# Performance work log

Hardware: AMD Instinct MI355X
Metric: run time of the kernel (lower is better)

## Reference

```python
import jax, jax.numpy as jnp
import numpy as np

N_NODES = 50000
N_GRAPHS = 2048
BN_EPS = 1e-5


def setup_inputs() -> dict:
    key = jax.random.key(0)
    ks = jax.random.split(key, 12)
    n_feat, dim, n_out, n_edges = 128, 128, 12, 800000
    x = jax.random.normal(ks[0], (N_NODES, n_feat), dtype=jnp.float32)
    edge_index = jax.random.randint(ks[1], (2, n_edges), 0, N_NODES, dtype=jnp.int32)
    batch = jnp.sort(jax.random.randint(ks[2], (N_NODES,), 0, N_GRAPHS, dtype=jnp.int32))
    def lin(k, fan_in, fan_out):
        bound = 1.0 / np.sqrt(fan_in)
        kw, kb = jax.random.split(k)
        W = jax.random.uniform(kw, (fan_in, fan_out), minval=-bound, maxval=bound, dtype=jnp.float32)
        b = jax.random.uniform(kb, (fan_out,), minval=-bound, maxval=bound, dtype=jnp.float32)
        return W, b
    W1, b1 = lin(ks[3], n_feat, dim)
    W2, b2 = lin(ks[4], dim, dim)
    gamma = jnp.ones((dim,), dtype=jnp.float32)
    beta = jnp.zeros((dim,), dtype=jnp.float32)
    Wf1, bf1 = lin(ks[5], dim, 2 * dim)
    Wf2, bf2 = lin(ks[6], 2 * dim, n_out)
    return {"x": x, "edge_index": edge_index, "batch": batch,
            "W1": W1, "b1": b1, "W2": W2, "b2": b2,
            "gamma": gamma, "beta": beta,
            "Wf1": Wf1, "bf1": bf1, "Wf2": Wf2, "bf2": bf2}


def reference(x, edge_index, batch, W1, b1, W2, b2, gamma, beta, Wf1, bf1, Wf2, bf2):
    src, dst = edge_index[0], edge_index[1]
    # GINConv (eps=0): h = nn1(x + sum_{j in N(i)} x_j), scatter-add at dst
    agg = jax.ops.segment_sum(x[src], dst, num_segments=N_NODES)  # [N, F]
    h = x + agg
    h = jax.nn.relu(h @ W1 + b1) @ W2 + b2  # nn1 MLP
    h = jax.nn.relu(h)
    # BatchNorm1d (training mode: batch statistics, biased variance)
    mean = jnp.mean(h, axis=0)
    var = jnp.mean((h - mean) ** 2, axis=0)
    h = (h - mean) * jax.lax.rsqrt(var + BN_EPS) * gamma + beta
    # global_add_pool over graphs
    g = jax.ops.segment_sum(h, batch, num_segments=N_GRAPHS)  # [G, dim]
    g = jax.nn.relu(g @ Wf1 + bf1)
    return g @ Wf2 + bf2  # [G, n_outputs]
```

## Files before the change

### kernel.cpp

```cpp
#include <hip/hip_runtime.h>

#define N_FEAT   128
#define N_GRAPHS 2048
#define BN_EPS   1e-5f
#define LDA      136
#define FHLD     132
#define EPB      4096

typedef __attribute__((ext_vector_type(8))) short  bf16x8;
typedef __attribute__((ext_vector_type(4))) float  f32x4;

__device__ __forceinline__ unsigned short f2bf(float f) {
    union { float f; unsigned int u; } c; c.f = f;
    unsigned int r = c.u + 0x7fffu + ((c.u >> 16) & 1u);
    return (unsigned short)(r >> 16);
}
__device__ __forceinline__ float bf2f(unsigned short h) {
    union { unsigned int u; float f; } c; c.u = ((unsigned int)h) << 16;
    return c.f;
}

__device__ __forceinline__ void acc8(float* a, int4 u) {
    unsigned int w[4] = {(unsigned int)u.x, (unsigned int)u.y,
                         (unsigned int)u.z, (unsigned int)u.w};
    #pragma unroll
    for (int k = 0; k < 4; ++k) {
        a[2 * k]     += __uint_as_float(w[k] << 16);
        a[2 * k + 1] += __uint_as_float(w[k] & 0xffff0000u);
    }
}

__global__ __launch_bounds__(256) void k_prep(const float* __restrict__ x,
                                              unsigned short* __restrict__ xb,
                                              int n8, int nbx,
                                              const float* __restrict__ W1,
                                              const float* __restrict__ W2,
                                              unsigned short* __restrict__ Wt1,
                                              unsigned short* __restrict__ Wt2,
                                              const int* __restrict__ batch,
                                              int* __restrict__ cnt, int n_nodes,
                                              int nbg,
                                              const int* __restrict__ dst,
                                              int* __restrict__ bcnt,
                                              int* __restrict__ btot,
                                              int n_edges, int nb2)
{
    int b = blockIdx.x, t = threadIdx.x;
    if (b < nbx) {
        int i = b * 256 + t;
        if (i >= n8) return;
        float4 a = ((const float4*)x)[i * 2];
        float4 c = ((const float4*)x)[i * 2 + 1];
        ushort4 u0, u1;
        u0.x = f2bf(a.x); u0.y = f2bf(a.y); u0.z = f2bf(a.z); u0.w = f2bf(a.w);
        u1.x = f2bf(c.x); u1.y = f2bf(c.y); u1.z = f2bf(c.z); u1.w = f2bf(c.w);
        ((ushort4*)xb)[i * 2]     = u0;
        ((ushort4*)xb)[i * 2 + 1] = u1;
    } else if (b < nbx + 128) {
        int i = (b - nbx) * 256 + t;
        int which = i >> 14;
        int k = (i >> 7) & 127;
        int c = i & 127;
        const float* W = which ? W2 : W1;
        unsigned short* O = which ? Wt2 : Wt1;
        O[c * 128 + k] = f2bf(W[k * 128 + c]);
    } else if (b < nbx + 128 + nbg) {
        int i = (b - nbx - 128) * 256 + t;
        if (i < n_nodes) atomicAdd(&cnt[batch[i]], 1);
    } else {
        __shared__ int lc[256];
        int blk = b - nbx - 128 - nbg;
        lc[t] = 0;
        __syncthreads();
        int base = blk * EPB;
        for (int i = t; i < EPB; i += 256) {
            int e = base + i;
            if (e < n_edges) atomicAdd(&lc[dst[e] >> 8], 1);
        }
        __syncthreads();
        bcnt[t * nb2 + blk] = lc[t];
        if (lc[t]) atomicAdd(&btot[t], lc[t]);
    }
}

__global__ __launch_bounds__(256) void k_bscan3(const int* __restrict__ bcnt,
                                                const int* __restrict__ btot,
                                                int* __restrict__ boff2, int nb2)
{
    __shared__ int s[256];
    int t = threadIdx.x, b = blockIdx.x;
    s[t] = (t < b) ? btot[t] : 0;
    __syncthreads();
    for (int o = 128; o > 0; o >>= 1) {
        if (t < o) s[t] += s[t + o];
        __syncthreads();
    }
    int base = s[0];
    __syncthreads();
    int c = (t < nb2) ? bcnt[b * nb2 + t] : 0;
    s[t] = c;
    __syncthreads();
    for (int o = 1; o < 256; o <<= 1) {
        int u = (t >= o) ? s[t - o] : 0;
        __syncthreads();
        s[t] += u;
        __syncthreads();
    }
    if (t < nb2) boff2[b * nb2 + t] = base + s[t] - c;
}

__global__ __launch_bounds__(256) void k_part(const int* __restrict__ src,
                                              const int* __restrict__ dst,
                                              const int* __restrict__ boff2,
                                              unsigned* __restrict__ epart,
                                              int n_edges, int nb2)
{
    __shared__ int lc[256];
    __shared__ int lofs[256];
    __shared__ unsigned buf[EPB];
    int t = threadIdx.x, blk = blockIdx.x;
    int base = blk * EPB;
    lc[t] = 0;
    __syncthreads();
    for (int i = t; i < EPB; i += 256) {
        int e = base + i;
        if (e < n_edges) atomicAdd(&lc[dst[e] >> 8], 1);
    }
    __syncthreads();
    int v = lc[t];
    lofs[t] = v;
    __syncthreads();
    for (int o = 1; o < 256; o <<= 1) {
        int u = (t >= o) ? lofs[t - o] : 0;
        __syncthreads();
        lofs[t] += u;
        __syncthreads();
    }
    int excl = lofs[t] - v;
    __syncthreads();
    lofs[t] = excl;
    lc[t] = 0;
    __syncthreads();
    for (int i = t; i < EPB; i += 256) {
        int e = base + i;
        if (e < n_edges) {
            int d = dst[e];
            int b = d >> 8;
            unsigned pack = ((unsigned)d << 16) | (unsigned)src[e];
            int r = atomicAdd(&lc[b], 1);
            buf[lofs[b] + r] = pack;
        }
    }
    __syncthreads();
    int total = min(EPB, n_edges - base);
    for (int i = t; i < total; i += 256) {
        unsigned pack = buf[i];
        int b = pack >> 24;
        int gpos = boff2[b * nb2 + blk] + (i - lofs[b]);
        epart[gpos] = pack;
    }
}

__global__ __launch_bounds__(256) void k_bfill(const unsigned* __restrict__ epart,
                                               const int* __restrict__ boff2,
                                               int* __restrict__ row_start,
                                               unsigned short* __restrict__ csr,
                                               int n_nodes, int nb2, int nbkt)
{
    __shared__ int cur[256];
    __shared__ int sc2[256];
    __shared__ unsigned short seg[8192];
    int t = threadIdx.x, b = blockIdx.x;
    int node0 = b * 256;
    int nodes = min(256, n_nodes - node0);
    int ebeg = boff2[(size_t)b * nb2];
    int eend = (b + 1 < nbkt) ? boff2[(size_t)(b + 1) * nb2] : boff2[(size_t)nbkt * nb2];

    cur[t] = 0;
    __syncthreads();
    for (int i = ebeg + t; i < eend; i += 256)
        atomicAdd(&cur[(epart[i] >> 16) - node0], 1);
    __syncthreads();
    int v = cur[t];
    sc2[t] = v;
    __syncthreads();
    for (int o = 1; o < 256; o <<= 1) {
        int u = (t >= o) ? sc2[t - o] : 0;
        __syncthreads();
        sc2[t] += u;
        __syncthreads();
    }
    int excl = sc2[t] - v;
    if (t < nodes) row_start[node0 + t] = ebeg + excl;
    if (b == nbkt - 1 && t == 0) row_start[n_nodes] = eend;
    __syncthreads();
    cur[t] = excl;
    __syncthreads();
    for (int i = ebeg + t; i < eend; i += 256) {
        unsigned pack = epart[i];
        int idx = (pack >> 16) - node0;
        int slot = atomicAdd(&cur[idx], 1);
        seg[slot] = (unsigned short)(pack & 0xffffu);
    }
    __syncthreads();
    int seglen = eend - ebeg;
    for (int i = t; i < seglen; i += 256) csr[ebeg + i] = seg[i];
}

__global__ __launch_bounds__(256) void k_gather(const unsigned short* __restrict__ xb,
                                                const unsigned short* __restrict__ csr,
                                                const int* __restrict__ row_start,
                                                unsigned short* __restrict__ A,
                                                int n_nodes)
{
    int node = blockIdx.x * 4 + (threadIdx.x >> 6);
    if (node >= n_nodes) return;
    int l = threadIdx.x & 63;
    int q = l >> 4;
    int lq = l & 15;
    const int4* xb4 = (const int4*)xb;
    int beg = row_start[node], end = row_start[node + 1];
    float a[8];
    #pragma unroll
    for (int i = 0; i < 8; ++i) a[i] = 0.f;

    int j = beg + q;
    for (; j + 12 < end; j += 16) {
        int s0 = csr[j], s1 = csr[j + 4], s2 = csr[j + 8], s3 = csr[j + 12];
        int4 u0 = xb4[(size_t)s0 * 16 + lq];
        int4 u1 = xb4[(size_t)s1 * 16 + lq];
        int4 u2 = xb4[(size_t)s2 * 16 + lq];
        int4 u3 = xb4[(size_t)s3 * 16 + lq];
        acc8(a, u0);
        acc8(a, u1);
        acc8(a, u2);
        acc8(a, u3);
    }
    for (; j < end; j += 4) {
        int4 u = xb4[(size_t)csr[j] * 16 + lq];
        acc8(a, u);
    }
    #pragma unroll
    for (int i = 0; i < 8; ++i) {
        a[i] += __shfl_xor(a[i], 16);
        a[i] += __shfl_xor(a[i], 32);
    }
    if (q == 0) {
        int4 uself = xb4[(size_t)node * 16 + lq];
        acc8(a, uself);
        unsigned int hw[4];
        #pragma unroll
        for (int i = 0; i < 4; ++i) {
            unsigned short h0 = f2bf(a[2 * i]);
            unsigned short h1 = f2bf(a[2 * i + 1]);
            hw[i] = (unsigned int)h0 | ((unsigned int)h1 << 16);
        }
        *(int4*)(A + (size_t)node * 128 + lq * 8) = make_int4(hw[0], hw[1], hw[2], hw[3]);
    }
}

__global__ __launch_bounds__(256) void k_mlp1_mfma(const unsigned short* __restrict__ A,
                                                   const unsigned short* __restrict__ Wt1,
                                                   const float* __restrict__ b1,
                                                   const unsigned short* __restrict__ Wt2,
                                                   const float* __restrict__ b2,
                                                   const int* __restrict__ batch,
                                                   float* __restrict__ g_raw,
                                                   float* __restrict__ partial,
                                                   int n_rows)
{
    __shared__ __align__(16) char smem[64 * FHLD * 4 + 256];
    unsigned short* sA = (unsigned short*)smem;

    int t = threadIdx.x;
    int wave = t >> 6, l = t & 63;
    int lr = l & 15;
    int lk = l >> 4;
    int row0 = blockIdx.x * 64;
    int col0 = wave * 32;

    #pragma unroll
    for (int it = 0; it < 4; ++it) {
        int idx = it * 256 + t;
        int r = idx >> 4, c8 = idx & 15;
        int gr = row0 + r;
        int4 vh = make_int4(0, 0, 0, 0);
        if (gr < n_rows) vh = ((const int4*)(A + (size_t)gr * 128))[c8];
        *(int4*)&sA[r * LDA + c8 * 8] = vh;
    }
    __syncthreads();

    f32x4 acc[4][2];
    #pragma unroll
    for (int m = 0; m < 4; ++m)
        #pragma unroll
        for (int n = 0; n < 2; ++n) acc[m][n] = (f32x4){0.f, 0.f, 0.f, 0.f};

    #pragma unroll
    for (int ks = 0; ks < 4; ++ks) {
        bf16x8 bfrag[2];
        #pragma unroll
        for (int n = 0; n < 2; ++n) {
            int c = col0 + n * 16 + lr;
            bfrag[n] = *(const bf16x8*)(Wt1 + (size_t)c * 128 + ks * 32 + lk * 8);
        }
        #pragma unroll
        for (int m = 0; m < 4; ++m) {
            bf16x8 ah = *(const bf16x8*)&sA[(m * 16 + lr) * LDA + ks * 32 + lk * 8];
            #pragma unroll
            for (int n = 0; n < 2; ++n)
                acc[m][n] = __builtin_amdgcn_mfma_f32_16x16x32_bf16(ah, bfrag[n], acc[m][n], 0, 0, 0);
        }
    }
    __syncthreads();

    #pragma unroll
    for (int n = 0; n < 2; ++n) {
        int c = col0 + n * 16 + lr;
        float bb = b1[c];
        #pragma unroll
        for (int m = 0; m < 4; ++m) {
            #pragma unroll
            for (int i = 0; i < 4; ++i) {
                int r = m * 16 + lk * 4 + i;
                sA[r * LDA + c] = f2bf(fmaxf(acc[m][n][i] + bb, 0.f));
            }
        }
    }
    __syncthreads();

    #pragma unroll
    for (int m = 0; m < 4; ++m)
        #pragma unroll
        for (int n = 0; n < 2; ++n) acc[m][n] = (f32x4){0.f, 0.f, 0.f, 0.f};

    #pragma unroll
    for (int ks = 0; ks < 4; ++ks) {
        bf16x8 bfrag[2];
        #pragma unroll
        for (int n = 0; n < 2; ++n) {
            int c = col0 + n * 16 + lr;
            bfrag[n] = *(const bf16x8*)(Wt2 + (size_t)c * 128 + ks * 32 + lk * 8);
        }
        #pragma unroll
        for (int m = 0; m < 4; ++m) {
            bf16x8 ah = *(const bf16x8*)&sA[(m * 16 + lr) * LDA + ks * 32 + lk * 8];
            #pragma unroll
            for (int n = 0; n < 2; ++n)
                acc[m][n] = __builtin_amdgcn_mfma_f32_16x16x32_bf16(ah, bfrag[n], acc[m][n], 0, 0, 0);
        }
    }

    float bb0 = b2[col0 + lr];
    float bb1 = b2[col0 + 16 + lr];
    int c0 = col0 + lr, c1 = col0 + 16 + lr;
    float v0s[4][4], v1s[4][4];
    float ps[2] = {0.f, 0.f}, pq[2] = {0.f, 0.f};
    #pragma unroll
    for (int m = 0; m < 4; ++m) {
        #pragma unroll
        for (int i = 0; i < 4; ++i) {
            int gr = row0 + m * 16 + lk * 4 + i;
            float v0 = fmaxf(acc[m][0][i] + bb0, 0.f);
            float v1 = fmaxf(acc[m][1][i] + bb1, 0.f);
            if (gr >= n_rows) { v0 = 0.f; v1 = 0.f; }
            v0s[m][i] = v0; v1s[m][i] = v1;
            ps[0] += v0; pq[0] += v0 * v0;
            ps[1] += v1; pq[1] += v1 * v1;
        }
    }
    #pragma unroll
    for (int n = 0; n < 2; ++n) {
        ps[n] += __shfl_xor(ps[n], 16); ps[n] += __shfl_xor(ps[n], 32);
        pq[n] += __shfl_xor(pq[n], 16); pq[n] += __shfl_xor(pq[n], 32);
    }
    if (lk == 0) {
        partial[(size_t)blockIdx.x * 256 + c0]       = ps[0];
        partial[(size_t)blockIdx.x * 256 + c1]       = ps[1];
        partial[(size_t)blockIdx.x * 256 + 128 + c0] = pq[0];
        partial[(size_t)blockIdx.x * 256 + 128 + c1] = pq[1];
    }

    __syncthreads();
    float (*fH)[FHLD] = (float (*)[FHLD])smem;
    int* sB = (int*)(smem + 64 * FHLD * sizeof(float));
    if (t < 64) sB[t] = (row0 + t < n_rows) ? batch[row0 + t] : -1;
    #pragma unroll
    for (int m = 0; m < 4; ++m) {
        #pragma unroll
        for (int i = 0; i < 4; ++i) {
            int r = m * 16 + lk * 4 + i;
            fH[r][c0] = v0s[m][i];
            fH[r][c1] = v1s[m][i];
        }
    }
    __syncthreads();

    {
        int c = t & 127;
        int rbeg = (t >> 7) * 32, rend = rbeg + 32;
        float a = 0.f;
        int bcur = sB[rbeg];
        for (int r = rbeg; r < rend; ++r) {
            int b = sB[r];
            if (b != bcur) {
                if (bcur >= 0) unsafeAtomicAdd(&g_raw[(size_t)bcur * 128 + c], a);
                a = 0.f; bcur = b;
            }
            a += fH[r][c];
        }
        if (bcur >= 0) unsafeAtomicAdd(&g_raw[(size_t)bcur * 128 + c], a);
    }
}

__global__ __launch_bounds__(256) void k_bnred(const float* __restrict__ partial,
                                               float* __restrict__ stats, int nblk)
{
    int j = threadIdx.x;
    float s = 0.f;
    for (int b = blockIdx.x; b < nblk; b += gridDim.x)
        s += partial[(size_t)b * 256 + j];
    unsafeAtomicAdd(&stats[j], s);
}

__global__ __launch_bounds__(256) void k_head(const float* __restrict__ g_raw,
                                              const int* __restrict__ cnt,
                                              const float* __restrict__ stats,
                                              const float* __restrict__ gamma,
                                              const float* __restrict__ beta,
                                              const float* __restrict__ Wf1,
                                              const float* __restrict__ bf1,
                                              const float* __restrict__ Wf2,
                                              const float* __restrict__ bf2,
                                              float* __restrict__ out, int n_rows)
{
    __shared__ float sg[4][128];
    __shared__ float sh[4][256];
    int t = threadIdx.x;
    int G0 = blockIdx.x * 4;
    if (t < 128) {
        float inv_n = 1.0f / (float)n_rows;
        float mean = stats[t] * inv_n;
        float var = stats[128 + t] * inv_n - mean * mean;
        float inv = rsqrtf(var + BN_EPS);
        float scale = gamma[t] * inv;
        float shift = beta[t] - mean * scale;
        #pragma unroll
        for (int gi = 0; gi < 4; ++gi) {
            float c = (float)cnt[G0 + gi];
            sg[gi][t] = g_raw[(size_t)(G0 + gi) * 128 + t] * scale + c * shift;
        }
    }
    __syncthreads();
    float a0 = bf1[t], a1 = a0, a2 = a0, a3 = a0;
    #pragma unroll 8
    for (int k = 0; k < 128; ++k) {
        float w = Wf1[k * 256 + t];
        a0 = fmaf(sg[0][k], w, a0);
        a1 = fmaf(sg[1][k], w, a1);
        a2 = fmaf(sg[2][k], w, a2);
        a3 = fmaf(sg[3][k], w, a3);
    }
    sh[0][t] = fmaxf(a0, 0.f);
    sh[1][t] = fmaxf(a1, 0.f);
    sh[2][t] = fmaxf(a2, 0.f);
    sh[3][t] = fmaxf(a3, 0.f);
    __syncthreads();
    if (t < 192) {
        int o = t >> 4, l = t & 15;
        float p0 = 0.f, p1 = 0.f, p2 = 0.f, p3 = 0.f;
        for (int k = l; k < 256; k += 16) {
            float w = Wf2[k * 12 + o];
            p0 += sh[0][k] * w;
            p1 += sh[1][k] * w;
            p2 += sh[2][k] * w;
            p3 += sh[3][k] * w;
        }
        #pragma unroll
        for (int m = 8; m >= 1; m >>= 1) {
            p0 += __shfl_xor(p0, m, 16);
            p1 += __shfl_xor(p1, m, 16);
            p2 += __shfl_xor(p2, m, 16);
            p3 += __shfl_xor(p3, m, 16);
        }
        if (l == 0) {
            float bb = bf2[o];
            out[(size_t)(G0 + 0) * 12 + o] = p0 + bb;
            out[(size_t)(G0 + 1) * 12 + o] = p1 + bb;
            out[(size_t)(G0 + 2) * 12 + o] = p2 + bb;
            out[(size_t)(G0 + 3) * 12 + o] = p3 + bb;
        }
    }
}

extern "C" void kernel_launch(void* const* d_in, const int* in_sizes, int n_in,
                              void* d_out, int out_size, void* d_ws, size_t ws_size,
                              hipStream_t stream)
{
    const float* x     = (const float*)d_in[0];
    const int*   ei    = (const int*)d_in[1];
    const int*   batch = (const int*)d_in[2];
    const float* W1    = (const float*)d_in[3];
    const float* b1    = (const float*)d_in[4];
    const float* W2    = (const float*)d_in[5];
    const float* b2    = (const float*)d_in[6];
    const float* gamma = (const float*)d_in[7];
    const float* beta  = (const float*)d_in[8];
    const float* Wf1   = (const float*)d_in[9];
    const float* bf1   = (const float*)d_in[10];
    const float* Wf2   = (const float*)d_in[11];
    const float* bf2   = (const float*)d_in[12];

    int n_nodes = in_sizes[0] / N_FEAT;
    int n_edges = in_sizes[1] / 2;
    const int* src = ei;
    const int* dst = ei + n_edges;

    char* ws = (char*)d_ws;
    size_t planeBytes = (size_t)n_nodes * N_FEAT * sizeof(unsigned short);
    size_t gBytes     = (size_t)N_GRAPHS * N_FEAT * sizeof(float);
    int nblk_m = (n_nodes + 63) / 64;
    int nb2    = (n_edges + EPB - 1) / EPB;
    int nbkt   = (n_nodes + 255) / 256;
    int nscan  = 256 * nb2;

    unsigned short* A   = (unsigned short*)ws;
    unsigned short* xb  = (unsigned short*)(ws + planeBytes);
    float* g_raw = (float*)(ws + 2 * planeBytes);
    float* stats = (float*)((char*)g_raw + gBytes);
    float* scSp  = stats + 256;
    int*   cnt   = (int*)(scSp + 256);
    int*   btot  = cnt + N_GRAPHS;
    unsigned short* Wt1 = (unsigned short*)(btot + 256);
    unsigned short* Wt2 = Wt1 + 128 * 128;
    float* partial = (float*)(Wt2 + 128 * 128);
    char* p = (char*)(partial + (size_t)nblk_m * 256);
    int* row_start = (int*)p;   p += (size_t)(n_nodes + 1) * sizeof(int);
    int* bcnt      = (int*)p;   p += (size_t)nscan * sizeof(int);
    int* boff2     = (int*)p;   p += (size_t)nscan * sizeof(int);
    unsigned* epart = (unsigned*)p;  p += (size_t)n_edges * sizeof(unsigned);
    unsigned short* csr = (unsigned short*)p;

    hipMemsetAsync(g_raw, 0,
                   gBytes + (256 + 256 + N_GRAPHS + 256) * sizeof(float), stream);

    int n8 = n_nodes * N_FEAT / 8;
    int nbx = (n8 + 255) / 256;
    int nbg = (n_nodes + 255) / 256;
    k_prep<<<nbx + 128 + nbg + nb2, 256, 0, stream>>>(x, xb, n8, nbx, W1, W2, Wt1, Wt2,
                                                      batch, cnt, n_nodes, nbg,
                                                      dst, bcnt, btot, n_edges, nb2);

    k_bscan3<<<256, 256, 0, stream>>>(bcnt, btot, boff2, nb2);
    k_part<<<nb2, 256, 0, stream>>>(src, dst, boff2, epart, n_edges, nb2);
    k_bfill<<<nbkt, 256, 0, stream>>>(epart, boff2, row_start, csr, n_nodes, nb2, nbkt);

    k_gather<<<(n_nodes + 3) / 4, 256, 0, stream>>>(xb, csr, row_start, A, n_nodes);

    k_mlp1_mfma<<<nblk_m, 256, 0, stream>>>(A, Wt1, b1, Wt2, b2, batch,
                                            g_raw, partial, n_nodes);

    k_bnred<<<64, 256, 0, stream>>>(partial, stats, nblk_m);
    k_head<<<N_GRAPHS / 4, 256, 0, stream>>>(g_raw, cnt, stats, gamma, beta,
                                             Wf1, bf1, Wf2, bf2, (float*)d_out, n_nodes);
}
```

Baseline: 122.0 us.

## Drop memset and atomic counters; derive counts by binary search and rescans

Removes the hipMemsetAsync by zeroing g_raw and stats inside extra blocks of the gather kernel. Graph node counts are now computed in the head kernel by binary search on the sorted batch array instead of atomic counting in prep. Bucket totals are recomputed per thread in the scan kernel by summing bcnt rows instead of atomics. The intent is to remove a launch and atomic traffic, in exchange for some redundant reads and a reliance on batch being sorted.

```diff
diff --git a/kernel.cpp b/kernel.cpp
--- a/kernel.cpp
+++ b/kernel.cpp
@@ -28,6 +28,12 @@
         a[2 * k]     += __uint_as_float(w[k] << 16);
         a[2 * k + 1] += __uint_as_float(w[k] & 0xffff0000u);
     }
+}
+
+__device__ __forceinline__ int lbound(const int* __restrict__ b, int n, int key) {
+    int lo = 0, hi = n;
+    while (lo < hi) { int m = (lo + hi) >> 1; if (b[m] < key) lo = m + 1; else hi = m; }
+    return lo;
 }
 
 __global__ __launch_bounds__(256) void k_prep(const float* __restrict__ x,
@@ -37,12 +43,8 @@
                                               const float* __restrict__ W2,
                                               unsigned short* __restrict__ Wt1,
                                               unsigned short* __restrict__ Wt2,
-                                              const int* __restrict__ batch,
-                                              int* __restrict__ cnt, int n_nodes,
-                                              int nbg,
                                               const int* __restrict__ dst,
                                               int* __restrict__ bcnt,
-                                              int* __restrict__ btot,
                                               int n_edges, int nb2)
 {
     int b = blockIdx.x, t = threadIdx.x;
@@ -64,12 +66,9 @@
         const float* W = which ? W2 : W1;
         unsigned short* O = which ? Wt2 : Wt1;
         O[c * 128 + k] = f2bf(W[k * 128 + c]);
-    } else if (b < nbx + 128 + nbg) {
-        int i = (b - nbx - 128) * 256 + t;
-        if (i < n_nodes) atomicAdd(&cnt[batch[i]], 1);
     } else {
         __shared__ int lc[256];
-        int blk = b - nbx - 128 - nbg;
+        int blk = b - nbx - 128;
         lc[t] = 0;
         __syncthreads();
         int base = blk * EPB;
@@ -79,17 +78,17 @@
         }
         __syncthreads();
         bcnt[t * nb2 + blk] = lc[t];
-        if (lc[t]) atomicAdd(&btot[t], lc[t]);
     }
 }
 
 __global__ __launch_bounds__(256) void k_bscan3(const int* __restrict__ bcnt,
-                                                const int* __restrict__ btot,
                                                 int* __restrict__ boff2, int nb2)
 {
     __shared__ int s[256];
     int t = threadIdx.x, b = blockIdx.x;
-    s[t] = (t < b) ? btot[t] : 0;
+    int rs = 0;
+    for (int i = 0; i < nb2; ++i) rs += bcnt[t * nb2 + i];
+    s[t] = (t < b) ? rs : 0;
     __syncthreads();
     for (int o = 128; o > 0; o >>= 1) {
         if (t < o) s[t] += s[t + o];
@@ -211,8 +210,15 @@
                                                 const unsigned short* __restrict__ csr,
                                                 const int* __restrict__ row_start,
                                                 unsigned short* __restrict__ A,
+                                                float* __restrict__ zbase,
+                                                int nz4, int gblocks,
                                                 int n_nodes)
 {
+    if (blockIdx.x >= gblocks) {
+        int zi = (blockIdx.x - gblocks) * 256 + threadIdx.x;
+        if (zi < nz4) ((float4*)zbase)[zi] = make_float4(0.f, 0.f, 0.f, 0.f);
+        return;
+    }
     int node = blockIdx.x * 4 + (threadIdx.x >> 6);
     if (node >= n_nodes) return;
     int l = threadIdx.x & 63;
@@ -424,7 +430,7 @@
 }
 
 __global__ __launch_bounds__(256) void k_head(const float* __restrict__ g_raw,
-                                              const int* __restrict__ cnt,
+                                              const int* __restrict__ batch,
                                               const float* __restrict__ stats,
                                               const float* __restrict__ gamma,
                                               const float* __restrict__ beta,
@@ -436,8 +442,11 @@
 {
     __shared__ float sg[4][128];
     __shared__ float sh[4][256];
+    __shared__ int sbnd[5];
     int t = threadIdx.x;
     int G0 = blockIdx.x * 4;
+    if (t < 5) sbnd[t] = lbound(batch, n_rows, G0 + t);
+    __syncthreads();
     if (t < 128) {
         float inv_n = 1.0f / (float)n_rows;
         float mean = stats[t] * inv_n;
@@ -447,7 +456,7 @@
         float shift = beta[t] - mean * scale;
         #pragma unroll
         for (int gi = 0; gi < 4; ++gi) {
-            float c = (float)cnt[G0 + gi];
+            float c = (float)(sbnd[gi + 1] - sbnd[gi]);
             sg[gi][t] = g_raw[(size_t)(G0 + gi) * 128 + t] * scale + c * shift;
         }
     }
@@ -528,10 +537,7 @@
     unsigned short* xb  = (unsigned short*)(ws + planeBytes);
     float* g_raw = (float*)(ws + 2 * planeBytes);
     float* stats = (float*)((char*)g_raw + gBytes);
-    float* scSp  = stats + 256;
-    int*   cnt   = (int*)(scSp + 256);
-    int*   btot  = cnt + N_GRAPHS;
-    unsigned short* Wt1 = (unsigned short*)(btot + 256);
+    unsigned short* Wt1 = (unsigned short*)(stats + 512);
     unsigned short* Wt2 = Wt1 + 128 * 128;
     float* partial = (float*)(Wt2 + 128 * 128);
     char* p = (char*)(partial + (size_t)nblk_m * 256);
@@ -541,26 +547,25 @@
     unsigned* epart = (unsigned*)p;  p += (size_t)n_edges * sizeof(unsigned);
     unsigned short* csr = (unsigned short*)p;
 
-    hipMemsetAsync(g_raw, 0,
-                   gBytes + (256 + 256 + N_GRAPHS + 256) * sizeof(float), stream);
-
     int n8 = n_nodes * N_FEAT / 8;
     int nbx = (n8 + 255) / 256;
-    int nbg = (n_nodes + 255) / 256;
-    k_prep<<<nbx + 128 + nbg + nb2, 256, 0, stream>>>(x, xb, n8, nbx, W1, W2, Wt1, Wt2,
-                                                      batch, cnt, n_nodes, nbg,
-                                                      dst, bcnt, btot, n_edges, nb2);
-
-    k_bscan3<<<256, 256, 0, stream>>>(bcnt, btot, boff2, nb2);
+    k_prep<<<nbx + 128 + nb2, 256, 0, stream>>>(x, xb, n8, nbx, W1, W2, Wt1, Wt2,
+                                                dst, bcnt, n_edges, nb2);
+
+    k_bscan3<<<256, 256, 0, stream>>>(bcnt, boff2, nb2);
     k_part<<<nb2, 256, 0, stream>>>(src, dst, boff2, epart, n_edges, nb2);
     k_bfill<<<nbkt, 256, 0, stream>>>(epart, boff2, row_start, csr, n_nodes, nb2, nbkt);
 
-    k_gather<<<(n_nodes + 3) / 4, 256, 0, stream>>>(xb, csr, row_start, A, n_nodes);
+    int gblocks = (n_nodes + 3) / 4;
+    int nz4 = (int)((gBytes + 512 * sizeof(float)) / 16);
+    int zblocks = (nz4 + 255) / 256;
+    k_gather<<<gblocks + zblocks, 256, 0, stream>>>(xb, csr, row_start, A,
+                                                    g_raw, nz4, gblocks, n_nodes);
 
     k_mlp1_mfma<<<nblk_m, 256, 0, stream>>>(A, Wt1, b1, Wt2, b2, batch,
                                             g_raw, partial, n_nodes);
 
     k_bnred<<<64, 256, 0, stream>>>(partial, stats, nblk_m);
-    k_head<<<N_GRAPHS / 4, 256, 0, stream>>>(g_raw, cnt, stats, gamma, beta,
+    k_head<<<N_GRAPHS / 4, 256, 0, stream>>>(g_raw, batch, stats, gamma, beta,
                                              Wf1, bf1, Wf2, bf2, (float*)d_out, n_nodes);
 }
```

New measurement: 135.8 us. +11.3%, slower.
